# Kernel tuning notes

Measured on AMD Instinct MI355X. Metric: run time of the kernel, lower is better.

The kernel has to match this reference:

```python
import jax, jax.numpy as jnp
import numpy as np

B, N, R = 4, 16, 64        # batch, permuted axis size, inner spatial size
M, S = N // 2, R * 2       # block count, block size


def _glorot(key, shape):
    fan_in, fan_out = shape[-2], shape[-1]
    lim = np.sqrt(6.0 / (fan_in + fan_out)).astype(np.float32)
    return jax.random.uniform(key, shape, jnp.float32, -lim, lim)


def setup_inputs() -> dict:
    key = jax.random.key(0)
    ks = jax.random.split(key, 10)
    inp = {
        "x": jax.random.normal(ks[0], (B, N, R, N, R, 2), jnp.float32),
        "perm_idx": jax.random.permutation(ks[1], N).astype(jnp.int32),
    }
    for i, name in enumerate(["hr1", "hi1", "hr2", "hi2", "hr3", "hi3", "hr4", "hi4"]):
        inp[name] = _glorot(ks[2 + i], (M, S, S))
    return inp


def _bilin(v, p_right, p_left):
    # v: (B, m, s, m, s). First contract the last s-axis against p_right's
    # block matmuls (block index = axis 3), then the axis-2 s-axis against
    # p_left's block matmuls (block index = axis 1).
    t = jnp.einsum('bmiaj,ajk->bmiak', v, p_right)
    return jnp.einsum('xbjci,bjk->xbkci', t, p_left)


def reference(x, perm_idx, hr1, hi1, hr2, hi2, hr3, hi3, hr4, hi4):
    m = x.shape[1] // 2
    s = x.shape[2] * 2
    n, r = m * 2, s // 2
    x = x.take(perm_idx, axis=1).take(perm_idx, axis=3)
    x = x.reshape((-1, m, s, m, s, 2))
    x_re, x_im = x[..., 0], x[..., 1]

    y_re = (_bilin(x_re, hr1, hr1) + _bilin(x_re, hi1, hi1)
            + _bilin(x_im, hi2, hr2) + _bilin(x_im, hr2, hi2))
    y_im = (_bilin(x_im, hr3, hr3) + _bilin(x_im, hi3, hi3)
            + _bilin(x_re, hi4, hr4) + _bilin(x_re, hr4, hi4))

    y = jnp.stack([y_re, y_im], axis=-1)
    return y.reshape((-1, n, r, n, r, 2))
```

## Files before the change

kernel.cpp:

```cpp
#include <hip/hip_runtime.h>
#include <hip/hip_bf16.h>
#include <stdint.h>

typedef __attribute__((ext_vector_type(8))) short bf16x8;
typedef __attribute__((ext_vector_type(4))) float f32x4;
typedef __attribute__((ext_vector_type(16))) float f32x16;

#define MFMA32(a, b, c) __builtin_amdgcn_mfma_f32_32x32x16_bf16((a), (b), (c), 0, 0, 0)

__device__ __forceinline__ unsigned short f2bf_rn(float f) {
    union { __bf16 b; unsigned short u; } v;
    v.b = (__bf16)f;
    return v.u;
}

__device__ __forceinline__ unsigned int pk2(float lo, float hi) {
    union { unsigned short s[2]; unsigned int u; } r;
    r.s[0] = f2bf_rn(lo); r.s[1] = f2bf_rn(hi);
    return r.u;
}

__device__ __forceinline__ void gload_lds16(const void* g, void* l) {
    __builtin_amdgcn_global_load_lds(
        (const __attribute__((address_space(1))) void*)g,
        (__attribute__((address_space(3))) void*)l, 16, 0, 0);
}

__global__ __launch_bounds__(256) void prep_h(
    const float* __restrict__ h0, const float* __restrict__ h1,
    const float* __restrict__ h2, const float* __restrict__ h3,
    const float* __restrict__ h4, const float* __restrict__ h5,
    const float* __restrict__ h6, const float* __restrict__ h7,
    unsigned short* __restrict__ ht)
{
    const float* hmap[8] = {h0, h1, h2, h3, h4, h5, h6, h7};
    const int wg = blockIdx.x;
    const int jblk = wg >> 2, qt = wg & 3;
    const float* src = hmap[jblk >> 3] + (jblk & 7) * 16384;
    unsigned short* dst = ht + jblk * 16384;
    __shared__ unsigned short tile[32 * 129];
    const int t = threadIdx.x;
    #pragma unroll
    for (int i = 0; i < 4; ++i) {
        int idx = t + 256 * i;
        int r = idx >> 3, kq = idx & 7;
        float4 v = *(const float4*)(src + r * 128 + qt * 32 + kq * 4);
        tile[(kq * 4 + 0) * 129 + r] = f2bf_rn(v.x);
        tile[(kq * 4 + 1) * 129 + r] = f2bf_rn(v.y);
        tile[(kq * 4 + 2) * 129 + r] = f2bf_rn(v.z);
        tile[(kq * 4 + 3) * 129 + r] = f2bf_rn(v.w);
    }
    __syncthreads();
    #pragma unroll
    for (int i = 0; i < 4; ++i) {
        int idx = t + 256 * i;
        int k = idx >> 5, rq = idx & 31;
        ushort4 o;
        o.x = tile[k * 129 + rq * 4 + 0];
        o.y = tile[k * 129 + rq * 4 + 1];
        o.z = tile[k * 129 + rq * 4 + 2];
        o.w = tile[k * 129 + rq * 4 + 3];
        *(ushort4*)(dst + (qt * 32 + k) * 128 + rq * 4) = o;
    }
}

__global__ __launch_bounds__(256, 1) void bilin_main(
    const float* __restrict__ x, const int* __restrict__ perm,
    const unsigned short* __restrict__ ht, float* __restrict__ out)
{
    const int wg = blockIdx.x;
    const int q = wg & 7, p = (wg >> 3) & 7, b = wg >> 6;
    const int tid = threadIdx.x;
    const int lane = tid & 63, wn = tid >> 6;
    const int l31 = lane & 31, hl = lane >> 5;

    __shared__ __align__(16) unsigned short smem[81920];
    unsigned short* xre_lds = smem;
    unsigned short* xim_lds = smem + 16384;
    unsigned short* llds = smem + 65536;

    constexpr int cseq[8]  = {0, 1, 6, 7, 2, 3, 4, 5};
    constexpr int rperm[8] = {0, 1, 3, 2, 4, 5, 7, 6};

    const int wubase = tid & ~63;
    auto stage_h = [&](unsigned short* dst, int blk) {
        const unsigned short* src = ht + blk * 16384;
        #pragma unroll
        for (int r = 0; r < 8; ++r) {
            const int idx = r * 256 + tid;
            const int row = idx >> 4, cin = idx & 15;
            gload_lds16(src + row * 128 + ((cin ^ (row & 15)) << 3),
                        dst + ((r * 256 + wubase) << 3));
        }
    };

    auto ldr = [&](const unsigned short* base, int row, int ch) -> bf16x8 {
        return *(const bf16x8*)(base + row * 128 + ((ch ^ (row & 15)) << 3));
    };

    auto stage_x_both = [&]() {
        #pragma unroll
        for (int i = 0; i < 8; ++i) {
            const int idx = i * 256 + tid;
            const int row = idx >> 4, cin = idx & 15;
            const int n1 = perm[2 * p + (row >> 6)];
            const int n2 = perm[2 * q + (cin >> 3)];
            const int r1 = row & 63, r2 = (cin & 7) * 8;
            const float* sp = x + ((size_t)((b * 16 + n1) * 64 + r1) * 1024
                                   + n2 * 64 + r2) * 2;
            float4 v0 = *(const float4*)(sp);
            float4 v1 = *(const float4*)(sp + 4);
            float4 v2 = *(const float4*)(sp + 8);
            float4 v3 = *(const float4*)(sp + 12);
            bf16x8 re, im;
            re[0] = (short)f2bf_rn(v0.x); re[1] = (short)f2bf_rn(v0.z);
            re[2] = (short)f2bf_rn(v1.x); re[3] = (short)f2bf_rn(v1.z);
            re[4] = (short)f2bf_rn(v2.x); re[5] = (short)f2bf_rn(v2.z);
            re[6] = (short)f2bf_rn(v3.x); re[7] = (short)f2bf_rn(v3.z);
            im[0] = (short)f2bf_rn(v0.y); im[1] = (short)f2bf_rn(v0.w);
            im[2] = (short)f2bf_rn(v1.y); im[3] = (short)f2bf_rn(v1.w);
            im[4] = (short)f2bf_rn(v2.y); im[5] = (short)f2bf_rn(v2.w);
            im[6] = (short)f2bf_rn(v3.y); im[7] = (short)f2bf_rn(v3.w);
            const int woff = row * 128 + ((cin ^ (row & 15)) << 3);
            *(bf16x8*)(xre_lds + woff) = re;
            *(bf16x8*)(xim_lds + woff) = im;
        }
    };

    bf16x8 xf[4][8];
    auto load_xf = [&](const unsigned short* plane) {
        #pragma unroll
        for (int m2 = 0; m2 < 4; ++m2)
            #pragma unroll
            for (int ks = 0; ks < 8; ++ks)
                xf[m2][ks] = ldr(plane, m2 * 32 + l31, 2 * ks + hl);
    };

    stage_h(smem + 32768, rperm[0] * 8 + q);
    stage_h(llds, 0 * 8 + p);
    stage_x_both();
    __syncthreads();
    load_xf(xre_lds);

    f32x16 yre[4], yim[4];
    #pragma unroll
    for (int i = 0; i < 4; ++i) {
        #pragma unroll
        for (int e = 0; e < 16; ++e) { yre[i][e] = 0.f; yim[i][e] = 0.f; }
    }

    #pragma unroll
    for (int cc = 0; cc < 8; ++cc) {
        const unsigned short* wb = smem + 32768 + (cc & 1) * 16384;

        if (cc < 7)
            stage_h(smem + 32768 + ((cc + 1) & 1) * 16384,
                    rperm[cseq[cc + 1]] * 8 + q);

        if (cc == 4) load_xf(xim_lds);

        bf16x8 wfr[8];
        #pragma unroll
        for (int ks = 0; ks < 8; ++ks)
            wfr[ks] = ldr(wb, wn * 32 + l31, 2 * ks + hl);
        f32x16 u[4];
        #pragma unroll
        for (int m2 = 0; m2 < 4; ++m2)
            #pragma unroll
            for (int e = 0; e < 16; ++e) u[m2][e] = 0.f;
        #pragma unroll
        for (int ks = 0; ks < 8; ++ks)
            #pragma unroll
            for (int m2 = 0; m2 < 4; ++m2)
                u[m2] = MFMA32(xf[m2][ks], wfr[ks], u[m2]);

        __syncthreads();

        bf16x8 lcur[4], lnxt[4];
        #pragma unroll
        for (int mt = 0; mt < 4; ++mt)
            lcur[mt] = ldr(llds, mt * 32 + l31, hl);
        #pragma unroll
        for (int mt = 0; mt < 4; ++mt)
            lnxt[mt] = ldr(llds, mt * 32 + l31, 2 + hl);

        union UF { unsigned int d[4]; bf16x8 v; };
        UF ufu[8];
        #pragma unroll
        for (int t = 0; t < 8; ++t) {
            const int f = t >> 1, qa = (t & 1) * 2, qb = qa + 1;
            unsigned int lo0 = pk2(u[f][4 * qa + 0], u[f][4 * qa + 1]);
            unsigned int lo1 = pk2(u[f][4 * qa + 2], u[f][4 * qa + 3]);
            unsigned int hi0 = pk2(u[f][4 * qb + 0], u[f][4 * qb + 1]);
            unsigned int hi1 = pk2(u[f][4 * qb + 2], u[f][4 * qb + 3]);
            unsigned int send0 = hl ? lo0 : hi0;
            unsigned int send1 = hl ? lo1 : hi1;
            unsigned int sx0 = (unsigned int)__shfl_xor((int)send0, 32);
            unsigned int sx1 = (unsigned int)__shfl_xor((int)send1, 32);
            ufu[t].d[0] = hl ? sx0 : lo0;
            ufu[t].d[1] = hl ? sx1 : lo1;
            ufu[t].d[2] = hl ? hi0 : sx0;
            ufu[t].d[3] = hl ? hi1 : sx1;
        }
        const bool isRe = (cc & 3) < 2;
        #pragma unroll
        for (int t = 0; t < 8; ++t) {
            #pragma unroll
            for (int mt = 0; mt < 4; ++mt) {
                if (isRe) yre[mt] = MFMA32(lcur[mt], ufu[t].v, yre[mt]);
                else      yim[mt] = MFMA32(lcur[mt], ufu[t].v, yim[mt]);
            }
            #pragma unroll
            for (int mt = 0; mt < 4; ++mt) lcur[mt] = lnxt[mt];
            if (t < 6) {
                #pragma unroll
                for (int mt = 0; mt < 4; ++mt)
                    lnxt[mt] = ldr(llds, mt * 32 + l31, 2 * (t + 2) + hl);
            }
        }

        __syncthreads();
        if (cc < 7)
            stage_h(llds, cseq[cc + 1] * 8 + p);
    }

    float2* o2 = (float2*)out;
    #pragma unroll
    for (int mt = 0; mt < 4; ++mt)
        #pragma unroll
        for (int j = 0; j < 16; ++j) {
            const int row = mt * 32 + (j & 3) + 8 * (j >> 2) + 4 * hl;
            float2 v;
            v.x = yre[mt][j];
            v.y = yim[mt][j];
            o2[(size_t)(b * 1024 + p * 128 + row) * 1024
               + q * 128 + wn * 32 + l31] = v;
        }
}

extern "C" void kernel_launch(void* const* d_in, const int* in_sizes, int n_in,
                              void* d_out, int out_size, void* d_ws, size_t ws_size,
                              hipStream_t stream) {
    const float* x  = (const float*)d_in[0];
    const int* perm = (const int*)d_in[1];
    unsigned short* htp = (unsigned short*)d_ws;

    hipLaunchKernelGGL(prep_h, dim3(256), dim3(256), 0, stream,
        (const float*)d_in[2], (const float*)d_in[3], (const float*)d_in[4],
        (const float*)d_in[5], (const float*)d_in[6], (const float*)d_in[7],
        (const float*)d_in[8], (const float*)d_in[9], htp);
    hipLaunchKernelGGL(bilin_main, dim3(256), dim3(256), 0, stream,
        x, perm, htp, (float*)d_out);
}
```

Baseline: 38.28 us.

## Reorder chunk schedule to finish real output first and store it early

Reorders the eight weight chunks so all real-part contributions come first and imaginary-part ones after, switching the resident x fragments between re/im planes as needed. Once the real accumulators are complete after chunk 3, they are written to global memory immediately, which overlaps that store with the remaining work and may let the compiler drop the live yre registers. The cost is an extra x-fragment reload (four switches instead of one) and strided scalar stores in place of float2 stores.

```diff
diff --git a/kernel.cpp b/kernel.cpp
--- a/kernel.cpp
+++ b/kernel.cpp
@@ -79,8 +79,8 @@
     unsigned short* xim_lds = smem + 16384;
     unsigned short* llds = smem + 65536;
 
-    constexpr int cseq[8]  = {0, 1, 6, 7, 2, 3, 4, 5};
-    constexpr int rperm[8] = {0, 1, 3, 2, 4, 5, 7, 6};
+    constexpr int cseq[8] = {0, 1, 2, 3, 6, 7, 4, 5};
+    constexpr int wseq[8] = {0, 1, 3, 2, 7, 6, 4, 5};
 
     const int wubase = tid & ~63;
     auto stage_h = [&](unsigned short* dst, int blk) {
@@ -136,8 +136,8 @@
                 xf[m2][ks] = ldr(plane, m2 * 32 + l31, 2 * ks + hl);
     };
 
-    stage_h(smem + 32768, rperm[0] * 8 + q);
-    stage_h(llds, 0 * 8 + p);
+    stage_h(smem + 32768, wseq[0] * 8 + q);
+    stage_h(llds, cseq[0] * 8 + p);
     stage_x_both();
     __syncthreads();
     load_xf(xre_lds);
@@ -155,9 +155,7 @@
 
         if (cc < 7)
             stage_h(smem + 32768 + ((cc + 1) & 1) * 16384,
-                    rperm[cseq[cc + 1]] * 8 + q);
-
-        if (cc == 4) load_xf(xim_lds);
+                    wseq[cc + 1] * 8 + q);
 
         bf16x8 wfr[8];
         #pragma unroll
@@ -202,7 +200,7 @@
             ufu[t].d[2] = hl ? hi0 : sx0;
             ufu[t].d[3] = hl ? hi1 : sx1;
         }
-        const bool isRe = (cc & 3) < 2;
+        const bool isRe = (cc < 4);
         #pragma unroll
         for (int t = 0; t < 8; ++t) {
             #pragma unroll
@@ -219,22 +217,32 @@
             }
         }
 
+        if (cc == 1 || cc == 5) load_xf(xim_lds);
+        if (cc == 3)            load_xf(xre_lds);
+
         __syncthreads();
         if (cc < 7)
             stage_h(llds, cseq[cc + 1] * 8 + p);
-    }
-
-    float2* o2 = (float2*)out;
+
+        if (cc == 3) {
+            #pragma unroll
+            for (int mt = 0; mt < 4; ++mt)
+                #pragma unroll
+                for (int j = 0; j < 16; ++j) {
+                    const int row = mt * 32 + (j & 3) + 8 * (j >> 2) + 4 * hl;
+                    out[((size_t)(b * 1024 + p * 128 + row) * 1024
+                         + q * 128 + wn * 32 + l31) * 2] = yre[mt][j];
+                }
+        }
+    }
+
     #pragma unroll
     for (int mt = 0; mt < 4; ++mt)
         #pragma unroll
         for (int j = 0; j < 16; ++j) {
             const int row = mt * 32 + (j & 3) + 8 * (j >> 2) + 4 * hl;
-            float2 v;
-            v.x = yre[mt][j];
-            v.y = yim[mt][j];
-            o2[(size_t)(b * 1024 + p * 128 + row) * 1024
-               + q * 128 + wn * 32 + l31] = v;
+            out[((size_t)(b * 1024 + p * 128 + row) * 1024
+                 + q * 128 + wn * 32 + l31) * 2 + 1] = yim[mt][j];
         }
 }
 
```

Measured after the change: 51.59 us. 1.35x slower.
